# Kernel optimization log

Hardware: AMD Instinct MI355X
Metric: run time of the kernel (lower is better)

## Reference

```python
import jax, jax.numpy as jnp
import numpy as np

D_MODEL = 1024
HIDDEN = 4096
N_EXPERTS = 8
LB_COEF = 0.01
B, N = 2, 2048


def setup_inputs() -> dict:
    key = jax.random.key(0)
    k_x, k_g, k_w1, k_w2 = jax.random.split(key, 4)
    s = 0.02
    return {
        "x": jax.random.normal(k_x, (B, N, D_MODEL), dtype=jnp.float32),
        "gate_w": jax.random.normal(k_g, (N_EXPERTS, D_MODEL), dtype=jnp.float32) * s,
        "w1": jax.random.normal(k_w1, (N_EXPERTS, HIDDEN, D_MODEL), dtype=jnp.float32) * s,  # torch Linear weight [out,in]
        "b1": jnp.zeros((N_EXPERTS, HIDDEN), dtype=jnp.float32),
        "w2": jax.random.normal(k_w2, (N_EXPERTS, D_MODEL, HIDDEN), dtype=jnp.float32) * s,
        "b2": jnp.zeros((N_EXPERTS, D_MODEL), dtype=jnp.float32),
    }


def reference(x, gate_w, w1, b1, w2, b2):
    # gate logits: Linear(d_model, E, bias=False)
    logits = jnp.einsum('bnd,ed->bne', x, gate_w)
    probs = jax.nn.softmax(logits, axis=-1)            # router_prob
    gate_scores = jnp.max(probs, axis=-1)              # top-1 prob [B,N]
    sel = jnp.argmax(probs, axis=-1)                   # selected expert [B,N]

    # load-balance aux loss
    onehot = jax.nn.one_hot(sel, N_EXPERTS, dtype=x.dtype)
    f = onehot.mean(axis=(0, 1))                       # fraction of tokens per expert
    P = probs.mean(axis=(0, 1))                        # mean router prob per expert
    aux_loss = LB_COEF * N_EXPERTS * jnp.sum(f * P)

    # dispatch: loop over fixed small expert count (structurally distinct weights)
    out = jnp.zeros_like(x)
    for e in range(N_EXPERTS):
        h = jax.nn.gelu(jnp.einsum('bnd,hd->bnh', x, w1[e]) + b1[e], approximate=False)
        y = jnp.einsum('bnh,dh->bnd', h, w2[e]) + b2[e]
        out = out + jnp.where((sel == e)[..., None], gate_scores[..., None] * y, jnp.zeros((), x.dtype))
    return out, aux_loss
```

## Files before the change

### kernel.cpp

```cpp
#include <hip/hip_runtime.h>
#include <math.h>

#define T_TOK 4096
#define DM 1024
#define HID 4096
#define NEXP 8
#define MAXT 39

typedef unsigned short u16;
typedef __attribute__((ext_vector_type(8))) short short8;
typedef __attribute__((ext_vector_type(4))) float f32x4;

__device__ __forceinline__ u16 f2bf(float f){
  unsigned u = __float_as_uint(f);
  u += 0x7FFF + ((u >> 16) & 1);
  return (u16)(u >> 16);
}

#define GATE_OFF   0u
#define CNT_OFF    16384u
#define LIST_OFF   16512u
#define PROBS_OFF  147584u
#define XB_OFF     278656u
#define H_OFF      8667264u
#define PART_OFF   42221696u

__device__ __forceinline__ void glds16(const void* g, void* l){
  __builtin_amdgcn_global_load_lds((const __attribute__((address_space(1))) void*)g,
                                   (__attribute__((address_space(3))) void*)l, 16, 0, 0);
}

__global__ void zero_cnt_kernel(int* cnt){
  if (threadIdx.x < NEXP) cnt[threadIdx.x] = 0;
}

__global__ __launch_bounds__(256) void gate_kernel(
    const float* __restrict__ x, const float* __restrict__ gw,
    float* __restrict__ gateo, int* __restrict__ cnt, int* __restrict__ list,
    float* __restrict__ probs, u16* __restrict__ xb)
{
  int tid = threadIdx.x;
  int lane = tid & 63;
  int w = tid >> 6;
  int t = blockIdx.x * 4 + w;

  const float4* x4 = (const float4*)(x + (size_t)t * DM);
  const float4* g4 = (const float4*)gw;

  float acc[8] = {0,0,0,0,0,0,0,0};
  #pragma unroll
  for (int i = 0; i < 4; i++){
    int p = i * 64 + lane;
    float4 xv = x4[p];
    ushort4 pk;
    pk.x = f2bf(xv.x); pk.y = f2bf(xv.y); pk.z = f2bf(xv.z); pk.w = f2bf(xv.w);
    *(ushort4*)&xb[(size_t)t * DM + (size_t)p * 4] = pk;
    #pragma unroll
    for (int e = 0; e < NEXP; e++){
      float4 gv = g4[e * 256 + p];
      acc[e] += xv.x * gv.x + xv.y * gv.y + xv.z * gv.z + xv.w * gv.w;
    }
  }
  #pragma unroll
  for (int e = 0; e < NEXP; e++){
    #pragma unroll
    for (int off = 32; off; off >>= 1)
      acc[e] += __shfl_xor(acc[e], off);
  }
  if (lane == 0){
    float mx = acc[0];
    #pragma unroll
    for (int e = 1; e < NEXP; e++) mx = fmaxf(mx, acc[e]);
    float p[8]; float s = 0.f;
    #pragma unroll
    for (int e = 0; e < NEXP; e++){ p[e] = expf(acc[e] - mx); s += p[e]; }
    float inv = 1.f / s;
    int be = 0; float bp = p[0];
    #pragma unroll
    for (int e = 1; e < NEXP; e++){ if (p[e] > bp){ bp = p[e]; be = e; } }
    #pragma unroll
    for (int e = 0; e < NEXP; e++) probs[(size_t)t * 8 + e] = p[e] * inv;
    gateo[t] = bp * inv;
    int pos = atomicAdd(&cnt[be], 1);
    list[be * T_TOK + pos] = t;
  }
}

__global__ __launch_bounds__(256) void aux_kernel(
    const float* __restrict__ probs, const int* __restrict__ cnt,
    float* __restrict__ aux_out)
{
  __shared__ float sm[256 * 8];
  int tid = threadIdx.x;
  float s[8] = {0,0,0,0,0,0,0,0};
  for (int i = 0; i < 16; i++){
    int t = i * 256 + tid;
    #pragma unroll
    for (int e = 0; e < 8; e++) s[e] += probs[(size_t)t * 8 + e];
  }
  #pragma unroll
  for (int e = 0; e < 8; e++) sm[tid * 8 + e] = s[e];
  __syncthreads();
  for (int st = 128; st; st >>= 1){
    if (tid < st){
      #pragma unroll
      for (int e = 0; e < 8; e++) sm[tid * 8 + e] += sm[(tid + st) * 8 + e];
    }
    __syncthreads();
  }
  if (tid == 0){
    float a = 0.f;
    #pragma unroll
    for (int e = 0; e < 8; e++){
      float f = (float)cnt[e] / (float)T_TOK;
      float P = sm[e] / (float)T_TOK;
      a += f * P;
    }
    aux_out[0] = 0.01f * (float)NEXP * a;
  }
}

template<int ASTR, int BSTR, int NTOT, int NT, int KS, bool PHASE2>
__global__ __launch_bounds__(256, 3) void ffn_gemm(
    const u16*  __restrict__ Aall,
    const float* __restrict__ Bf,
    const float* __restrict__ bias,
    const int*  __restrict__ cnt,
    const int*  __restrict__ list,
    u16*  __restrict__ hOut,
    float* __restrict__ pOut)
{
  int bid = blockIdx.x;
  int nt = bid % NT;
  int r1 = bid / NT;
  int t  = r1 % MAXT;
  int sk = r1 / MAXT;

  int e = -1, mt = 0, accT = 0;
  #pragma unroll
  for (int i = 0; i < NEXP; i++){
    int nti = (cnt[i] + 127) >> 7;
    if (e < 0 && t < accT + nti){ e = i; mt = t - accT; }
    accT += nti;
  }
  if (e < 0) return;
  int ne = cnt[e];
  int m0 = mt * 128;
  const int* lst = list + e * T_TOK;
  int n0 = nt * 128;
  int koff = sk * (KS * 64);

  __shared__ u16 As[8192];
  __shared__ u16 Bs[8192];

  int tid  = threadIdx.x;
  int lane = tid & 63;
  int w    = tid >> 6;
  int wm = w >> 1, wn = w & 1;
  int fr = lane & 15, fq = lane >> 4;

  const u16* aS[4]; int aDst[4];
  #pragma unroll
  for (int i = 0; i < 4; i++){
    int seg = w * 4 + i;
    int r   = seg * 8 + (lane >> 3);
    int g   = (lane & 7) ^ (r & 7);
    int mrow = m0 + r; if (mrow > ne - 1) mrow = ne - 1;
    aS[i] = Aall + (size_t)lst[mrow] * ASTR + koff + g * 8;
    aDst[i] = seg * 512;
  }

  const float* bS[4]; int bDst[4];
  #pragma unroll
  for (int i = 0; i < 4; i++){
    int c = i * 256 + tid;
    int r = c >> 3, sl = c & 7;
    int g = sl ^ (r & 7);
    bS[i] = Bf + ((size_t)e * NTOT + n0 + r) * BSTR + koff + g * 8;
    bDst[i] = r * 64 + sl * 8;
  }

  f32x4 acc[4][4];
  #pragma unroll
  for (int m = 0; m < 4; m++)
    #pragma unroll
    for (int n = 0; n < 4; n++)
      acc[m][n] = (f32x4){0.f, 0.f, 0.f, 0.f};

  float4 br0[4], br1[4];
  #pragma unroll
  for (int i = 0; i < 4; i++){
    const float4* s = (const float4*)bS[i];
    br0[i] = s[0]; br1[i] = s[1];
  }

  for (int ks = 0; ks < KS; ++ks){
    if (ks) __syncthreads();
    size_t ko = (size_t)ks * 64;
    #pragma unroll
    for (int i = 0; i < 4; i++) glds16(aS[i] + ko, &As[aDst[i]]);
    #pragma unroll
    for (int i = 0; i < 4; i++){
      uint4 pk;
      pk.x = (unsigned)f2bf(br0[i].x) | ((unsigned)f2bf(br0[i].y) << 16);
      pk.y = (unsigned)f2bf(br0[i].z) | ((unsigned)f2bf(br0[i].w) << 16);
      pk.z = (unsigned)f2bf(br1[i].x) | ((unsigned)f2bf(br1[i].y) << 16);
      pk.w = (unsigned)f2bf(br1[i].z) | ((unsigned)f2bf(br1[i].w) << 16);
      *(uint4*)&Bs[bDst[i]] = pk;
    }
    if (ks + 1 < KS){
      #pragma unroll
      for (int i = 0; i < 4; i++){
        const float4* s = (const float4*)(bS[i] + (ks + 1) * 64);
        br0[i] = s[0]; br1[i] = s[1];
      }
    }
    __syncthreads();
    #pragma unroll
    for (int kc = 0; kc < 2; kc++){
      short8 afr[4], bfr[4];
      #pragma unroll
      for (int m = 0; m < 4; m++){
        int row  = wm * 64 + m * 16 + fr;
        int slot = (kc * 4 + fq) ^ (row & 7);
        afr[m] = *(const short8*)&As[row * 64 + slot * 8];
      }
      #pragma unroll
      for (int n = 0; n < 4; n++){
        int row  = wn * 64 + n * 16 + fr;
        int slot = (kc * 4 + fq) ^ (row & 7);
        bfr[n] = *(const short8*)&Bs[row * 64 + slot * 8];
      }
      #pragma unroll
      for (int m = 0; m < 4; m++)
        #pragma unroll
        for (int n = 0; n < 4; n++)
          acc[m][n] = __builtin_amdgcn_mfma_f32_16x16x32_bf16(afr[m], bfr[n], acc[m][n], 0, 0, 0);
    }
  }

  #pragma unroll
  for (int n = 0; n < 4; n++){
    int col = n0 + wn * 64 + n * 16 + fr;
    float bv = bias[(size_t)e * NTOT + col];
    if (PHASE2 && sk != 0) bv = 0.f;
    #pragma unroll
    for (int m = 0; m < 4; m++){
      int rbase = m0 + wm * 64 + m * 16 + fq * 4;
      f32x4 v = acc[m][n];
      #pragma unroll
      for (int i = 0; i < 4; i++){
        int mrow = rbase + i;
        if (mrow < ne){
          int tok = lst[mrow];
          float val = v[i] + bv;
          if (PHASE2){
            pOut[((size_t)sk * T_TOK + tok) * DM + col] = val;
          } else {
            float gl = 0.5f * val * (1.0f + erff(val * 0.70710678118654752f));
            hOut[(size_t)tok * HID + col] = f2bf(gl);
          }
        }
      }
    }
  }
}

__global__ __launch_bounds__(256) void reduce_kernel(
    const float* __restrict__ part, const float* __restrict__ gate,
    float* __restrict__ out)
{
  size_t i = (size_t)blockIdx.x * 256 + threadIdx.x;
  constexpr size_t S = (size_t)T_TOK * DM / 4;
  const float4* p = (const float4*)part;
  float4 a = p[i], b = p[i + S], c = p[i + 2 * S], d = p[i + 3 * S];
  float g = gate[i >> 8];
  float4 o;
  o.x = (a.x + b.x + c.x + d.x) * g;
  o.y = (a.y + b.y + c.y + d.y) * g;
  o.z = (a.z + b.z + c.z + d.z) * g;
  o.w = (a.w + b.w + c.w + d.w) * g;
  ((float4*)out)[i] = o;
}

extern "C" void kernel_launch(void* const* d_in, const int* in_sizes, int n_in,
                              void* d_out, int out_size, void* d_ws, size_t ws_size,
                              hipStream_t stream) {
  const float* x   = (const float*)d_in[0];
  const float* gw  = (const float*)d_in[1];
  const float* w1  = (const float*)d_in[2];
  const float* b1  = (const float*)d_in[3];
  const float* w2  = (const float*)d_in[4];
  const float* b2  = (const float*)d_in[5];

  char* ws = (char*)d_ws;
  float* gateo = (float*)(ws + GATE_OFF);
  int*   cnt   = (int*)  (ws + CNT_OFF);
  int*   list  = (int*)  (ws + LIST_OFF);
  float* probs = (float*)(ws + PROBS_OFF);
  u16*   xb    = (u16*)  (ws + XB_OFF);
  u16*   h     = (u16*)  (ws + H_OFF);
  float* part  = (float*)(ws + PART_OFF);

  float* out = (float*)d_out;
  float* aux = out + (size_t)T_TOK * DM;

  hipLaunchKernelGGL(zero_cnt_kernel, dim3(1), dim3(64), 0, stream, cnt);
  hipLaunchKernelGGL(gate_kernel, dim3(T_TOK / 4), dim3(256), 0, stream,
                     x, gw, gateo, cnt, list, probs, xb);
  hipLaunchKernelGGL(aux_kernel, dim3(1), dim3(256), 0, stream, probs, cnt, aux);

  hipLaunchKernelGGL((ffn_gemm<DM, DM, HID, 32, 16, false>),
                     dim3(MAXT * 32), dim3(256), 0, stream,
                     xb, w1, b1, cnt, list, h, (float*)nullptr);
  hipLaunchKernelGGL((ffn_gemm<HID, HID, DM, 8, 16, true>),
                     dim3(4 * MAXT * 8), dim3(256), 0, stream,
                     h, w2, b2, cnt, list, (u16*)nullptr, part);
  hipLaunchKernelGGL(reduce_kernel, dim3(T_TOK * DM / 4 / 256), dim3(256), 0, stream,
                     part, gateo, out);
}
```

Baseline: 302.1 us.

## Remap GEMM block indices into 4x8 tile groups for L2 reuse across XCDs

Replaces the linear block-to-tile mapping in both expert GEMMs with a grouped scheme. Each group of 32 blocks covers 4 M-tiles by 8 N-tiles (or K-splits in phase 2) of one expert, and the low 3 bits of the block id are interleaved so consecutive blocks land in different groups, apparently to match the 8-XCD round-robin dispatch. The aim is for blocks that share A rows and B weight tiles to run on the same XCD, improving L2 hit rates on weight and activation loads. It launches a fixed 2048 blocks, many of which exit early, and relies on the assumed XCD assignment pattern.

After: 311.9 us. 1.03x slower.

```diff
diff --git a/kernel.cpp b/kernel.cpp
--- a/kernel.cpp
+++ b/kernel.cpp
@@ -5,7 +5,6 @@
 #define DM 1024
 #define HID 4096
 #define NEXP 8
-#define MAXT 39
 
 typedef unsigned short u16;
 typedef __attribute__((ext_vector_type(8))) short short8;
@@ -120,7 +119,7 @@
   }
 }
 
-template<int ASTR, int BSTR, int NTOT, int NT, int KS, bool PHASE2>
+template<int ASTR, int BSTR, int NTOT, int KS, bool PHASE2>
 __global__ __launch_bounds__(256, 3) void ffn_gemm(
     const u16*  __restrict__ Aall,
     const float* __restrict__ Bf,
@@ -131,22 +130,31 @@
     float* __restrict__ pOut)
 {
   int bid = blockIdx.x;
-  int nt = bid % NT;
-  int r1 = bid / NT;
-  int t  = r1 % MAXT;
-  int sk = r1 / MAXT;
-
-  int e = -1, mt = 0, accT = 0;
+  int x  = bid & 7;
+  int r  = bid >> 3;
+  int j  = r & 31;
+  int Wq = r >> 5;
+  int W  = Wq * 8 + x;
+  int dm = j >> 3, dn = j & 7;
+
+  int e = -1, g = 0, c = 0, Te = 0, accW = 0;
   #pragma unroll
   for (int i = 0; i < NEXP; i++){
-    int nti = (cnt[i] + 127) >> 7;
-    if (e < 0 && t < accT + nti){ e = i; mt = t - accT; }
-    accT += nti;
+    int ti = (cnt[i] + 127) >> 7;
+    int wi = ((ti + 3) >> 2) * 4;
+    if (e < 0 && W < accW + wi){
+      int Wl = W - accW; e = i; g = Wl >> 2; c = Wl & 3; Te = ti;
+    }
+    accW += wi;
   }
   if (e < 0) return;
+  int mt = g * 4 + dm;
+  if (mt >= Te) return;
   int ne = cnt[e];
   int m0 = mt * 128;
   const int* lst = list + e * T_TOK;
+  int nt = PHASE2 ? dn : (c * 8 + dn);
+  int sk = PHASE2 ? c : 0;
   int n0 = nt * 128;
   int koff = sk * (KS * 64);
 
@@ -163,21 +171,21 @@
   #pragma unroll
   for (int i = 0; i < 4; i++){
     int seg = w * 4 + i;
-    int r   = seg * 8 + (lane >> 3);
-    int g   = (lane & 7) ^ (r & 7);
-    int mrow = m0 + r; if (mrow > ne - 1) mrow = ne - 1;
-    aS[i] = Aall + (size_t)lst[mrow] * ASTR + koff + g * 8;
+    int rr  = seg * 8 + (lane >> 3);
+    int gg  = (lane & 7) ^ (rr & 7);
+    int mrow = m0 + rr; if (mrow > ne - 1) mrow = ne - 1;
+    aS[i] = Aall + (size_t)lst[mrow] * ASTR + koff + gg * 8;
     aDst[i] = seg * 512;
   }
 
   const float* bS[4]; int bDst[4];
   #pragma unroll
   for (int i = 0; i < 4; i++){
-    int c = i * 256 + tid;
-    int r = c >> 3, sl = c & 7;
-    int g = sl ^ (r & 7);
-    bS[i] = Bf + ((size_t)e * NTOT + n0 + r) * BSTR + koff + g * 8;
-    bDst[i] = r * 64 + sl * 8;
+    int cc = i * 256 + tid;
+    int rr = cc >> 3, sl = cc & 7;
+    int gg = sl ^ (rr & 7);
+    bS[i] = Bf + ((size_t)e * NTOT + n0 + rr) * BSTR + koff + gg * 8;
+    bDst[i] = rr * 64 + sl * 8;
   }
 
   f32x4 acc[4][4];
@@ -310,11 +318,11 @@
                      x, gw, gateo, cnt, list, probs, xb);
   hipLaunchKernelGGL(aux_kernel, dim3(1), dim3(256), 0, stream, probs, cnt, aux);
 
-  hipLaunchKernelGGL((ffn_gemm<DM, DM, HID, 32, 16, false>),
-                     dim3(MAXT * 32), dim3(256), 0, stream,
+  hipLaunchKernelGGL((ffn_gemm<DM, DM, HID, 16, false>),
+                     dim3(2048), dim3(256), 0, stream,
                      xb, w1, b1, cnt, list, h, (float*)nullptr);
-  hipLaunchKernelGGL((ffn_gemm<HID, HID, DM, 8, 16, true>),
-                     dim3(4 * MAXT * 8), dim3(256), 0, stream,
+  hipLaunchKernelGGL((ffn_gemm<HID, HID, DM, 16, true>),
+                     dim3(2048), dim3(256), 0, stream,
                      h, w2, b2, cnt, list, (u16*)nullptr, part);
   hipLaunchKernelGGL(reduce_kernel, dim3(T_TOK * DM / 4 / 256), dim3(256), 0, stream,
                      part, gateo, out);
```

## Convert w2 to bf16 in extra GEMM1 blocks and use direct LDS loads in GEMM2

Applied to the files above, without the earlier changes.

GEMM1 gains 512 extra blocks that convert the fp32 w2 weights to bf16 in workspace while the main GEMM1 tiles run. GEMM2 then loads both operands from bf16 with global_load_lds, with no register-staged fp32 conversion of B. The aim is to hide the weight conversion behind GEMM1 and make GEMM2's inner loop cheaper. The cost is an extra pass that reads all of w2 and writes a bf16 copy on every call, competing with GEMM1 for bandwidth.

Result: no change. 296.2 us, median of 2 (-1.9%).

```diff
diff --git a/kernel.cpp b/kernel.cpp
--- a/kernel.cpp
+++ b/kernel.cpp
@@ -6,6 +6,7 @@
 #define HID 4096
 #define NEXP 8
 #define MAXT 39
+#define NG1  1248
 
 typedef unsigned short u16;
 typedef __attribute__((ext_vector_type(8))) short short8;
@@ -24,6 +25,7 @@
 #define XB_OFF     278656u
 #define H_OFF      8667264u
 #define PART_OFF   42221696u
+#define W2B_OFF    109330560u
 
 __device__ __forceinline__ void glds16(const void* g, void* l){
   __builtin_amdgcn_global_load_lds((const __attribute__((address_space(1))) void*)g,
@@ -120,21 +122,38 @@
   }
 }
 
-template<int ASTR, int BSTR, int NTOT, int NT, int KS, bool PHASE2>
-__global__ __launch_bounds__(256, 3) void ffn_gemm(
+__global__ __launch_bounds__(256, 3) void ffn_gemm1(
     const u16*  __restrict__ Aall,
     const float* __restrict__ Bf,
     const float* __restrict__ bias,
     const int*  __restrict__ cnt,
     const int*  __restrict__ list,
     u16*  __restrict__ hOut,
-    float* __restrict__ pOut)
+    const float* __restrict__ w2,
+    u16*  __restrict__ w2b)
 {
   int bid = blockIdx.x;
+  int tid = threadIdx.x;
+
+  if (bid >= NG1){
+    const size_t TOT = (size_t)NEXP * DM * HID / 8;
+    size_t stride = (size_t)512 * 256;
+    for (size_t g = (size_t)(bid - NG1) * 256 + tid; g < TOT; g += stride){
+      const float4* s = (const float4*)w2 + g * 2;
+      float4 a = s[0], c = s[1];
+      uint4 p;
+      p.x = (unsigned)f2bf(a.x) | ((unsigned)f2bf(a.y) << 16);
+      p.y = (unsigned)f2bf(a.z) | ((unsigned)f2bf(a.w) << 16);
+      p.z = (unsigned)f2bf(c.x) | ((unsigned)f2bf(c.y) << 16);
+      p.w = (unsigned)f2bf(c.z) | ((unsigned)f2bf(c.w) << 16);
+      ((uint4*)w2b)[g] = p;
+    }
+    return;
+  }
+
+  constexpr int NT = 32, KS = 16;
   int nt = bid % NT;
-  int r1 = bid / NT;
-  int t  = r1 % MAXT;
-  int sk = r1 / MAXT;
+  int t  = bid / NT;
 
   int e = -1, mt = 0, accT = 0;
   #pragma unroll
@@ -148,12 +167,10 @@
   int m0 = mt * 128;
   const int* lst = list + e * T_TOK;
   int n0 = nt * 128;
-  int koff = sk * (KS * 64);
 
   __shared__ u16 As[8192];
   __shared__ u16 Bs[8192];
 
-  int tid  = threadIdx.x;
   int lane = tid & 63;
   int w    = tid >> 6;
   int wm = w >> 1, wn = w & 1;
@@ -163,21 +180,21 @@
   #pragma unroll
   for (int i = 0; i < 4; i++){
     int seg = w * 4 + i;
-    int r   = seg * 8 + (lane >> 3);
-    int g   = (lane & 7) ^ (r & 7);
-    int mrow = m0 + r; if (mrow > ne - 1) mrow = ne - 1;
-    aS[i] = Aall + (size_t)lst[mrow] * ASTR + koff + g * 8;
+    int rr  = seg * 8 + (lane >> 3);
+    int gg  = (lane & 7) ^ (rr & 7);
+    int mrow = m0 + rr; if (mrow > ne - 1) mrow = ne - 1;
+    aS[i] = Aall + (size_t)lst[mrow] * DM + gg * 8;
     aDst[i] = seg * 512;
   }
 
   const float* bS[4]; int bDst[4];
   #pragma unroll
   for (int i = 0; i < 4; i++){
-    int c = i * 256 + tid;
-    int r = c >> 3, sl = c & 7;
-    int g = sl ^ (r & 7);
-    bS[i] = Bf + ((size_t)e * NTOT + n0 + r) * BSTR + koff + g * 8;
-    bDst[i] = r * 64 + sl * 8;
+    int cc = i * 256 + tid;
+    int rr = cc >> 3, sl = cc & 7;
+    int gg = sl ^ (rr & 7);
+    bS[i] = Bf + ((size_t)e * HID + n0 + rr) * DM + gg * 8;
+    bDst[i] = rr * 64 + sl * 8;
   }
 
   f32x4 acc[4][4];
@@ -242,8 +259,7 @@
   #pragma unroll
   for (int n = 0; n < 4; n++){
     int col = n0 + wn * 64 + n * 16 + fr;
-    float bv = bias[(size_t)e * NTOT + col];
-    if (PHASE2 && sk != 0) bv = 0.f;
+    float bv = bias[(size_t)e * HID + col];
     #pragma unroll
     for (int m = 0; m < 4; m++){
       int rbase = m0 + wm * 64 + m * 16 + fq * 4;
@@ -254,12 +270,116 @@
         if (mrow < ne){
           int tok = lst[mrow];
           float val = v[i] + bv;
-          if (PHASE2){
-            pOut[((size_t)sk * T_TOK + tok) * DM + col] = val;
-          } else {
-            float gl = 0.5f * val * (1.0f + erff(val * 0.70710678118654752f));
-            hOut[(size_t)tok * HID + col] = f2bf(gl);
-          }
+          float gl = 0.5f * val * (1.0f + erff(val * 0.70710678118654752f));
+          hOut[(size_t)tok * HID + col] = f2bf(gl);
+        }
+      }
+    }
+  }
+}
+
+__global__ __launch_bounds__(256, 3) void ffn_gemm2(
+    const u16*  __restrict__ Aall,
+    const u16*  __restrict__ Bb,
+    const float* __restrict__ bias,
+    const int*  __restrict__ cnt,
+    const int*  __restrict__ list,
+    float* __restrict__ pOut)
+{
+  constexpr int NT = 8, KS = 16;
+  int bid = blockIdx.x;
+  int nt = bid % NT;
+  int r1 = bid / NT;
+  int t  = r1 % MAXT;
+  int sk = r1 / MAXT;
+
+  int e = -1, mt = 0, accT = 0;
+  #pragma unroll
+  for (int i = 0; i < NEXP; i++){
+    int nti = (cnt[i] + 127) >> 7;
+    if (e < 0 && t < accT + nti){ e = i; mt = t - accT; }
+    accT += nti;
+  }
+  if (e < 0) return;
+  int ne = cnt[e];
+  int m0 = mt * 128;
+  const int* lst = list + e * T_TOK;
+  int n0 = nt * 128;
+  int koff = sk * (KS * 64);
+
+  __shared__ u16 As[8192];
+  __shared__ u16 Bs[8192];
+
+  int tid  = threadIdx.x;
+  int lane = tid & 63;
+  int w    = tid >> 6;
+  int wm = w >> 1, wn = w & 1;
+  int fr = lane & 15, fq = lane >> 4;
+
+  const u16* aS[4]; const u16* bS[4]; int dst[4];
+  #pragma unroll
+  for (int i = 0; i < 4; i++){
+    int seg = w * 4 + i;
+    int r   = seg * 8 + (lane >> 3);
+    int g   = (lane & 7) ^ (r & 7);
+    int mrow = m0 + r; if (mrow > ne - 1) mrow = ne - 1;
+    aS[i] = Aall + (size_t)lst[mrow] * HID + koff + g * 8;
+    bS[i] = Bb + (size_t)e * DM * HID + (size_t)(n0 + r) * HID + koff + g * 8;
+    dst[i] = seg * 512;
+  }
+
+  f32x4 acc[4][4];
+  #pragma unroll
+  for (int m = 0; m < 4; m++)
+    #pragma unroll
+    for (int n = 0; n < 4; n++)
+      acc[m][n] = (f32x4){0.f, 0.f, 0.f, 0.f};
+
+  for (int ks = 0; ks < KS; ++ks){
+    if (ks) __syncthreads();
+    size_t ko = (size_t)ks * 64;
+    #pragma unroll
+    for (int i = 0; i < 4; i++) glds16(aS[i] + ko, &As[dst[i]]);
+    #pragma unroll
+    for (int i = 0; i < 4; i++) glds16(bS[i] + ko, &Bs[dst[i]]);
+    __syncthreads();
+    #pragma unroll
+    for (int kc = 0; kc < 2; kc++){
+      short8 afr[4], bfr[4];
+      #pragma unroll
+      for (int m = 0; m < 4; m++){
+        int row  = wm * 64 + m * 16 + fr;
+        int slot = (kc * 4 + fq) ^ (row & 7);
+        afr[m] = *(const short8*)&As[row * 64 + slot * 8];
+      }
+      #pragma unroll
+      for (int n = 0; n < 4; n++){
+        int row  = wn * 64 + n * 16 + fr;
+        int slot = (kc * 4 + fq) ^ (row & 7);
+        bfr[n] = *(const short8*)&Bs[row * 64 + slot * 8];
+      }
+      #pragma unroll
+      for (int m = 0; m < 4; m++)
+        #pragma unroll
+        for (int n = 0; n < 4; n++)
+          acc[m][n] = __builtin_amdgcn_mfma_f32_16x16x32_bf16(afr[m], bfr[n], acc[m][n], 0, 0, 0);
+    }
+  }
+
+  #pragma unroll
+  for (int n = 0; n < 4; n++){
+    int col = n0 + wn * 64 + n * 16 + fr;
+    float bv = (sk == 0) ? bias[(size_t)e * DM + col] : 0.f;
+    #pragma unroll
+    for (int m = 0; m < 4; m++){
+      int rbase = m0 + wm * 64 + m * 16 + fq * 4;
+      f32x4 v = acc[m][n];
+      #pragma unroll
+      for (int i = 0; i < 4; i++){
+        int mrow = rbase + i;
+        if (mrow < ne){
+          int tok = lst[mrow];
+          pOut[((size_t)sk * T_TOK + tok) * DM + col] = v[i] + bv;
         }
       }
     }
@@ -301,6 +421,7 @@
   u16*   xb    = (u16*)  (ws + XB_OFF);
   u16*   h     = (u16*)  (ws + H_OFF);
   float* part  = (float*)(ws + PART_OFF);
+  u16*   w2b   = (u16*)  (ws + W2B_OFF);
 
   float* out = (float*)d_out;
   float* aux = out + (size_t)T_TOK * DM;
@@ -310,12 +431,10 @@
                      x, gw, gateo, cnt, list, probs, xb);
   hipLaunchKernelGGL(aux_kernel, dim3(1), dim3(256), 0, stream, probs, cnt, aux);
 
-  hipLaunchKernelGGL((ffn_gemm<DM, DM, HID, 32, 16, false>),
-                     dim3(MAXT * 32), dim3(256), 0, stream,
-                     xb, w1, b1, cnt, list, h, (float*)nullptr);
-  hipLaunchKernelGGL((ffn_gemm<HID, HID, DM, 8, 16, true>),
-                     dim3(4 * MAXT * 8), dim3(256), 0, stream,
-                     h, w2, b2, cnt, list, (u16*)nullptr, part);
+  hipLaunchKernelGGL(ffn_gemm1, dim3(NG1 + 512), dim3(256), 0, stream,
+                     xb, w1, b1, cnt, list, h, w2, w2b);
+  hipLaunchKernelGGL(ffn_gemm2, dim3(4 * MAXT * 8), dim3(256), 0, stream,
+                     h, w2b, b2, cnt, list, part);
   hipLaunchKernelGGL(reduce_kernel, dim3(T_TOK * DM / 4 / 256), dim3(256), 0, stream,
                      part, gateo, out);
 }
```
